# Kernel optimization log

Hardware: AMD Instinct MI355X
Metric: run time of the kernel (lower is better)

The kernel has to match this reference:

```python
import jax, jax.numpy as jnp
import numpy as np
from jax import lax

H = 160; W = 160
D_MODEL = 128; D_INNER = 512; D_STATE = 256; NHEADS = 16; HEADDIM = 32
D_CONV = 4; CHUNK = 64
CONV_DIM = D_INNER + 2 * D_STATE            # 1024
D_IN_PROJ = 2 * D_INNER + 2 * D_STATE + NHEADS  # 1552
EPS = 1e-5


def setup_inputs() -> dict:
    key = jax.random.key(0)
    ks = jax.random.split(key, 8)
    nrm = lambda k, s, sc: jax.random.normal(k, s, jnp.float32) * sc
    return {
        "x": jax.random.normal(ks[0], (1, 3, H, W), jnp.float32),
        "fc0_w": nrm(ks[1], (D_MODEL, 3), 0.3),
        "fc0_b": jnp.zeros((D_MODEL,), jnp.float32),
        "in_proj_w": nrm(ks[2], (D_IN_PROJ, D_MODEL), D_MODEL ** -0.5),
        "conv_w": nrm(ks[3], (CONV_DIM, D_CONV), 0.3),
        "conv_b": jnp.zeros((CONV_DIM,), jnp.float32),
        "dt_bias": jnp.log(jnp.expm1(jax.random.uniform(ks[4], (NHEADS,), minval=0.001, maxval=0.1))),
        "A_log": jnp.log(jax.random.uniform(ks[5], (NHEADS,), minval=1.0, maxval=16.0)),
        "D": jnp.ones((NHEADS,), jnp.float32),
        "norm_w": jnp.ones((D_INNER,), jnp.float32),
        "out_proj_w": nrm(ks[6], (D_MODEL, D_INNER), D_INNER ** -0.5),
        "fc1_w": nrm(ks[7], (D_MODEL, H * W), (H * W) ** -0.5),
        "fc1_b": jnp.zeros((D_MODEL,), jnp.float32),
    }


def segsum(x):
    # x: (..., T) -> (..., T, T) with out[i,j] = sum_{j < d <= i} x[d], -inf above diag
    T = x.shape[-1]
    strict = jnp.tril(jnp.ones((T, T), dtype=bool), -1)
    xx = jnp.where(strict, x[..., :, None], 0.0)
    cs = jnp.cumsum(xx, axis=-2)
    keep = jnp.tril(jnp.ones((T, T), dtype=bool))
    return jnp.where(keep, cs, -jnp.inf)


def ssd(xh, A, Bm, Cm):
    # xh: (b,l,h,p) already multiplied by dt; A: (b,l,h) = dt*A_head; Bm,Cm: (b,l,n) (ngroups=1)
    b, l, h, p = xh.shape
    n = Bm.shape[-1]
    c, q = l // CHUNK, CHUNK
    xh = xh.reshape(b, c, q, h, p)
    A = A.reshape(b, c, q, h).transpose(0, 3, 1, 2)          # (b,h,c,q)
    Bm = Bm.reshape(b, c, q, n)
    Cm = Cm.reshape(b, c, q, n)
    A_cs = jnp.cumsum(A, axis=-1)                            # (b,h,c,q)
    Lmat = jnp.exp(segsum(A))                                # (b,h,c,q,q)
    # intra-chunk (quadratic attention-like) term
    Y_diag = jnp.einsum('bcln,bcsn,bhcls,bcshp->bclhp', Cm, Bm, Lmat, xh)
    # per-chunk final states
    decay = jnp.exp(A_cs[..., -1:] - A_cs)                   # (b,h,c,q)
    states = jnp.einsum('bcln,bhcl,bclhp->bchpn', Bm, decay, xh)
    # inter-chunk recurrence: state entering each chunk
    a_tot = jnp.exp(A_cs[..., -1])                           # (b,h,c)
    def step(carry, inp):
        a_c, s_c = inp                                       # (b,h), (b,h,p,n)
        return a_c[..., None, None] * carry + s_c, carry
    _, states_in = lax.scan(step, jnp.zeros((b, h, p, n), xh.dtype),
                            (jnp.moveaxis(a_tot, 2, 0), jnp.moveaxis(states, 1, 0)))
    states_in = jnp.moveaxis(states_in, 0, 1)                # (b,c,h,p,n)
    Y_off = jnp.einsum('bcln,bchpn,bhcl->bclhp', Cm, states_in, jnp.exp(A_cs))
    return (Y_diag + Y_off).reshape(b, l, h, p)


def _forward(x, fc0_w, fc0_b, in_proj_w, conv_w, conv_b, dt_bias, A_log, D,
             norm_w, out_proj_w, fc1_w, fc1_b):
    b = x.shape[0]
    hw = H * W
    # bidirectional pixel flattening
    x1 = x.transpose(0, 2, 3, 1).reshape(b, hw, 3)
    x2 = x[:, :, ::-1, ::-1].transpose(0, 2, 3, 1).reshape(b, hw, 3)
    xc = jnp.concatenate([x1, x2], axis=1)                   # (b, 2*hw, 3)
    u = xc @ fc0_w.T + fc0_b                                 # (b, L, 128)
    L = u.shape[1]
    # Mamba2 in_proj
    zxbcdt = u @ in_proj_w.T                                 # (b, L, 1552)
    z = zxbcdt[..., :D_INNER]
    xBC = zxbcdt[..., D_INNER:D_INNER + CONV_DIM]
    dt = jax.nn.softplus(zxbcdt[..., D_INNER + CONV_DIM:] + dt_bias)  # (b, L, 16)
    # causal depthwise conv1d + silu
    conv = lax.conv_general_dilated(xBC.transpose(0, 2, 1), conv_w[:, None, :],
                                    (1,), [(D_CONV - 1, 0)],
                                    feature_group_count=CONV_DIM,
                                    dimension_numbers=('NCH', 'OIH', 'NCH'))
    xBC = jax.nn.silu(conv + conv_b[None, :, None]).transpose(0, 2, 1)
    xh = xBC[..., :D_INNER].reshape(b, L, NHEADS, HEADDIM)
    Bm = xBC[..., D_INNER:D_INNER + D_STATE]
    Cm = xBC[..., D_INNER + D_STATE:]
    A = -jnp.exp(A_log)                                      # (16,)
    Y = ssd(xh * dt[..., None], dt * A, Bm, Cm)
    Y = Y + D[None, None, :, None] * xh                      # skip connection
    y = Y.reshape(b, L, D_INNER)
    # gated RMSNorm (norm_before_gate=False)
    y = y * jax.nn.silu(z)
    y = y * lax.rsqrt(jnp.mean(y * y, axis=-1, keepdims=True) + EPS) * norm_w
    out = y @ out_proj_w.T                                   # (b, L, 128)
    # second half of sequence, mean over feature dim (AdaptiveAvgPool1d(1))
    half = out[:, hw:, :].mean(axis=-1)                      # (b, hw)
    return half @ fc1_w.T + fc1_b                            # (b, 128)


def reference(x, fc0_w, fc0_b, in_proj_w, conv_w, conv_b, dt_bias, A_log, D,
              norm_w, out_proj_w, fc1_w, fc1_b):
    return _forward(x, fc0_w, fc0_b, in_proj_w, conv_w, conv_b, dt_bias, A_log,
                    D, norm_w, out_proj_w, fc1_w, fc1_b)
```

## Files before the change

### kernel.cpp

```cpp
#include <hip/hip_runtime.h>

#define H_ 160
#define W_ 160
#define HW 25600
#define L_ 51200
#define DM 128
#define DI 512
#define DS 256
#define NH 16
#define HD 32
#define CONVD 1024
#define DIP 1552
#define NCH 800
#define NCH2 400
#define HPB 8
#define KSL 32
#define CPS 13
#define EPSV 1e-5f

typedef __attribute__((ext_vector_type(8))) short bf16x8;
typedef __attribute__((ext_vector_type(8))) unsigned short us8;
typedef __attribute__((ext_vector_type(4))) unsigned short us4;
typedef __attribute__((ext_vector_type(4))) float f32x4;
#define MFMA16(a,b,c) __builtin_amdgcn_mfma_f32_16x16x32_bf16(a,b,c,0,0,0)

__device__ __forceinline__ float b2f(unsigned short u){
  union{unsigned int i; float f;} v; v.i = ((unsigned int)u) << 16; return v.f;
}
__device__ __forceinline__ unsigned short f2b(float f){
  union{unsigned int i; float f;} v; v.f = f;
  unsigned int r = v.i + 0x7fffu + ((v.i >> 16) & 1u);
  return (unsigned short)(r >> 16);
}

__global__ void k_coef(const float* __restrict__ opw, const float* __restrict__ nw,
                       float* __restrict__ coef){
  int i = blockIdx.x * blockDim.x + threadIdx.x;
  if (i >= DI) return;
  float s = 0.f;
  for (int j = 0; j < DM; ++j) s += opw[j * DI + i];
  coef[i] = (s / (float)DM) * nw[i];
}

__global__ __launch_bounds__(256) void k_qtab(const float* __restrict__ ipw,
    const float* __restrict__ fw, const float* __restrict__ fb, float* __restrict__ q){
  int j = blockIdx.x * 256 + threadIdx.x;
  if (j >= DIP) return;
  const float* wr = ipw + (size_t)j * DM;
  float s0 = 0.f, s1 = 0.f, s2 = 0.f, sb = 0.f;
  for (int k = 0; k < DM; ++k){
    float w = wr[k];
    s0 += w * fw[k*3+0]; s1 += w * fw[k*3+1]; s2 += w * fw[k*3+2]; sb += w * fb[k];
  }
  reinterpret_cast<float4*>(q)[j] = make_float4(s0, s1, s2, sb);
}

__device__ __forceinline__ void xrow(const float* __restrict__ x, int l, float* o){
  int i, j;
  if (l < HW){ i = l / W_; j = l % W_; }
  else { int l2 = l - HW; i = (H_ - 1) - l2 / W_; j = (W_ - 1) - l2 % W_; }
  int p = i * W_ + j;
  o[0] = x[p]; o[1] = x[HW + p]; o[2] = x[2*HW + p];
}

__global__ __launch_bounds__(256) void k_fused(const float* __restrict__ x,
    const float* __restrict__ q, const float* __restrict__ cw, const float* __restrict__ cb,
    const float* __restrict__ dt_bias,
    unsigned short* __restrict__ g, unsigned short* __restrict__ xbc, float* __restrict__ dtb){
  int r0 = blockIdx.x * 32;
  int tid = threadIdx.x;
  {
    int c8 = tid & 127, lg = tid >> 7;
    const float4* qv8 = reinterpret_cast<const float4*>(q) + DI + c8 * 8;
    const float4* wv8 = reinterpret_cast<const float4*>(cw) + c8 * 8;
    const float4* cb2 = reinterpret_cast<const float4*>(cb) + c8 * 2;
    float4 bias0 = cb2[0], bias1 = cb2[1];
    float biasv[8] = {bias0.x,bias0.y,bias0.z,bias0.w,bias1.x,bias1.y,bias1.z,bias1.w};
    for (int it = 0; it < 4; ++it){
      int lbase = r0 + (it * 2 + lg) * 4;
      float xv[7][3], vf[7];
      #pragma unroll
      for (int k = 0; k < 7; ++k){
        int l = lbase - 3 + k;
        if (l >= 0){ xrow(x, l, xv[k]); vf[k] = 1.f; }
        else { xv[k][0] = xv[k][1] = xv[k][2] = 0.f; vf[k] = 0.f; }
      }
      unsigned int ow[4][4];
      #pragma unroll
      for (int e = 0; e < 8; ++e){
        float4 qv = qv8[e];
        float raw[7];
        #pragma unroll
        for (int k = 0; k < 7; ++k)
          raw[k] = vf[k]*qv.w + xv[k][0]*qv.x + xv[k][1]*qv.y + xv[k][2]*qv.z;
        float4 wv = wv8[e];
        float bias = biasv[e];
        #pragma unroll
        for (int rr = 0; rr < 4; ++rr){
          float acc = bias + raw[rr]*wv.x + raw[rr+1]*wv.y + raw[rr+2]*wv.z + raw[rr+3]*wv.w;
          float s = acc / (1.f + __expf(-acc));
          unsigned int b = f2b(s);
          if (e & 1) ow[rr][e >> 1] |= b << 16;
          else       ow[rr][e >> 1] = b;
        }
      }
      #pragma unroll
      for (int rr = 0; rr < 4; ++rr){
        uint4 o; o.x = ow[rr][0]; o.y = ow[rr][1]; o.z = ow[rr][2]; o.w = ow[rr][3];
        *reinterpret_cast<uint4*>(xbc + (size_t)(lbase + rr) * CONVD + c8 * 8) = o;
      }
    }
  }
  if (r0 >= HW){
    int c8g = tid & 63;
    const float4* qv8 = reinterpret_cast<const float4*>(q) + c8g * 8;
    for (int it = 0; it < 8; ++it){
      int row = it * 4 + (tid >> 6);
      int l = r0 + row;
      float xv[3]; xrow(x, l, xv);
      unsigned int ow[4];
      #pragma unroll
      for (int e = 0; e < 8; ++e){
        float4 qv = qv8[e];
        float raw = qv.w + xv[0]*qv.x + xv[1]*qv.y + xv[2]*qv.z;
        float s = raw / (1.f + __expf(-raw));
        unsigned int b = f2b(s);
        if (e & 1) ow[e >> 1] |= b << 16;
        else       ow[e >> 1] = b;
      }
      uint4 o; o.x = ow[0]; o.y = ow[1]; o.z = ow[2]; o.w = ow[3];
      *reinterpret_cast<uint4*>(g + (size_t)(l - HW) * DI + c8g * 8) = o;
    }
  }
  {
    int row = tid >> 3, h2 = (tid & 7) * 2;
    int l = r0 + row;
    float xv[3]; xrow(x, l, xv);
    #pragma unroll
    for (int e = 0; e < 2; ++e){
      int h = h2 + e;
      float4 qv = reinterpret_cast<const float4*>(q)[DI + CONVD + h];
      float raw = qv.w + xv[0]*qv.x + xv[1]*qv.y + xv[2]*qv.z + dt_bias[h];
      float sp = (raw > 20.f) ? raw : log1pf(__expf(raw));
      dtb[(size_t)l * NH + h] = sp;
    }
  }
}

__global__ void k_csum(const float* __restrict__ dtb, const float* __restrict__ A_log,
                       float* __restrict__ Scs){
  int idx = blockIdx.x * 256 + threadIdx.x;
  if (idx >= NCH2 * NH) return;
  int c = idx >> 4, h = idx & 15;
  float Ah = -__expf(A_log[h]);
  float s = 0.f;
  const float* p = dtb + (size_t)c * 64 * NH + h;
  for (int t = 0; t < 64; ++t) s += p[t * NH];
  Scs[idx] = s * Ah;
}

__global__ __launch_bounds__(256) void k_cpre(const float* __restrict__ Scs,
    float* __restrict__ chunkpre, float* __restrict__ Ttot){
  __shared__ float segs[256];
  int tid = threadIdx.x;
  int h = tid & 15, seg = tid >> 4;
  int c0 = seg * 25;
  float v[25];
  float s = 0.f;
  #pragma unroll
  for (int j = 0; j < 25; ++j){ v[j] = Scs[(c0 + j) * NH + h]; s += v[j]; }
  segs[seg * 16 + h] = s;
  __syncthreads();
  float excl = 0.f;
  for (int s2 = 0; s2 < seg; ++s2) excl += segs[s2 * 16 + h];
  float run = excl;
  #pragma unroll
  for (int j = 0; j < 25; ++j){ chunkpre[(c0 + j) * NH + h] = run; run += v[j]; }
  if (seg == 15) Ttot[h] = run;
}

__global__ __launch_bounds__(256) void k_carry(const unsigned short* __restrict__ xbc,
    const float* __restrict__ dtb, const float* __restrict__ A_log,
    const float* __restrict__ chunkpre, const float* __restrict__ Ttot,
    float* __restrict__ part){
  __shared__ char U[37120];
  unsigned short* Bs = (unsigned short*)U;
  char* xwT = U + 32768;
  float* wcs = (float*)(U + 36864);
  int h = blockIdx.x & 15, ks = blockIdx.x >> 4;
  int tid = threadIdx.x, lane = tid & 63, wv = tid >> 6;
  int kg = lane >> 4, l15 = lane & 15;
  int c0 = ks * CPS, cend = min(c0 + CPS, NCH2);
  float Ah = -__expf(A_log[h]);
  float Tt = Ttot[h];
  f32x4 sacc[2][4];
  #pragma unroll
  for (int mt = 0; mt < 2; ++mt)
    #pragma unroll
    for (int nt = 0; nt < 4; ++nt) sacc[mt][nt] = (f32x4){0.f,0.f,0.f,0.f};
  for (int c = c0; c < cend; ++c){
    int l0 = c * 64;
    __syncthreads();
    #pragma unroll
    for (int it = 0; it < 8; ++it){
      int r = (tid >> 5) + 8 * it, c8 = tid & 31;
      uint4 v = *reinterpret_cast<const uint4*>(xbc + (size_t)(l0 + r) * CONVD + DI + c8 * 8);
      *reinterpret_cast<uint4*>((char*)Bs + ((r * 512 + c8 * 16) ^ ((r & 7) << 4))) = v;
    }
    if (wv == 0){
      float d = dtb[(size_t)(l0 + lane) * NH + h] * Ah;
      #pragma unroll
      for (int off = 1; off < 64; off <<= 1){
        float o = __shfl_up(d, off, 64);
        if (lane >= off) d += o;
      }
      wcs[lane] = __expf(Tt - chunkpre[c * NH + h] - d);
    }
    __syncthreads();
    {
      int t = lane, pb = wv;
      float w = wcs[t] * dtb[(size_t)(l0 + t) * NH + h];
      us8 x8 = *reinterpret_cast<const us8*>(xbc + (size_t)(l0 + t) * CONVD + h * HD + pb * 8);
      #pragma unroll
      for (int e = 0; e < 8; ++e){
        int pp = pb * 8 + e;
        *reinterpret_cast<unsigned short*>(xwT + ((pp * 128 + t * 2) ^ ((pp & 7) << 4))) = f2b(b2f(x8[e]) * w);
      }
    }
    __syncthreads();
    #pragma unroll
    for (int s = 0; s < 2; ++s){
      bf16x8 bfr[4];
      #pragma unroll
      for (int nt = 0; nt < 4; ++nt){
        int n = wv * 64 + nt * 16 + l15;
        bf16x8 f;
        #pragma unroll
        for (int e = 0; e < 8; ++e){
          int t = s * 32 + kg * 8 + e;
          f[e] = *reinterpret_cast<const short*>((char*)Bs + ((t * 512 + n * 2) ^ ((t & 7) << 4)));
        }
        bfr[nt] = f;
      }
      #pragma unroll
      for (int mt = 0; mt < 2; ++mt){
        int pr = mt * 16 + l15;
        bf16x8 a = *reinterpret_cast<const bf16x8*>(xwT + ((pr * 128 + (s*32 + kg*8) * 2) ^ ((pr & 7) << 4)));
        #pragma unroll
        for (int nt = 0; nt < 4; ++nt) sacc[mt][nt] = MFMA16(a, bfr[nt], sacc[mt][nt]);
      }
    }
  }
  float* pb2 = part + ((size_t)(ks * NH + h)) * HD * DS;
  #pragma unroll
  for (int mt = 0; mt < 2; ++mt)
    #pragma unroll
    for (int nt = 0; nt < 4; ++nt)
      #pragma unroll
      for (int r = 0; r < 4; ++r)
        pb2[(mt * 16 + kg * 4 + r) * DS + wv * 64 + nt * 16 + l15] = sacc[mt][nt][r];
}

__global__ __launch_bounds__(256) void k_carryred(const float* __restrict__ part,
                                                  float* __restrict__ carry){
  int idx = blockIdx.x * 256 + threadIdx.x;
  float s = 0.f;
  #pragma unroll 8
  for (int ks = 0; ks < KSL; ++ks) s += part[(size_t)ks * 131072 + idx];
  carry[idx] = s;
}

__global__ __launch_bounds__(256) void k_chunk(const unsigned short* __restrict__ xbc,
    const float* __restrict__ dtb, const float* __restrict__ A_log,
    unsigned short* __restrict__ states, float* __restrict__ atot,
    float* __restrict__ ecs, unsigned short* __restrict__ ydiag){
  __shared__ char U[65536];
  __shared__ float dts[64 * HPB];
  __shared__ float Acs[HPB * 64];
  unsigned short* Bs = (unsigned short*)U;
  unsigned short* Cs = (unsigned short*)(U + 32768);
  char* Mb  = U;
  char* xdT = U + 8192;
  char* xwT = U + 12288;
  unsigned short* stageS = (unsigned short*)(U + 16384);
  unsigned short* stageY = (unsigned short*)(U + 33280);
  int cl = blockIdx.x >> 1, hg = blockIdx.x & 1;
  int hbase = hg * HPB;
  int c = NCH2 + cl, l0 = c * 64;
  int tid = threadIdx.x, lane = tid & 63, wv = tid >> 6;
  int kg = lane >> 4, l15 = lane & 15;

  for (int i = tid; i < 64 * HPB; i += 256){
    int t = i >> 3, hh = i & 7;
    dts[i] = dtb[(size_t)(l0 + t) * NH + hbase + hh];
  }
  #pragma unroll
  for (int it = 0; it < 8; ++it){
    int r = (tid >> 5) + 8 * it, c8 = tid & 31;
    uint4 v = *reinterpret_cast<const uint4*>(xbc + (size_t)(l0 + r) * CONVD + DI + c8 * 8);
    *reinterpret_cast<uint4*>((char*)Bs + ((r * 512 + c8 * 16) ^ ((r & 7) << 4))) = v;
    uint4 v2 = *reinterpret_cast<const uint4*>(xbc + (size_t)(l0 + r) * CONVD + DI + DS + c8 * 8);
    *reinterpret_cast<uint4*>((char*)Cs + ((r * 512 + c8 * 16) ^ ((r & 7) << 4))) = v2;
  }
  __syncthreads();
  if (tid < HPB){
    int hh = tid; float Ah = -__expf(A_log[hbase + hh]); float s = 0.f;
    for (int t = 0; t < 64; ++t){ s += dts[t*HPB + hh] * Ah; Acs[hh*64 + t] = s; }
    atot[c * NH + hbase + hh] = __expf(s);
  }
  bf16x8 bst[8];
  #pragma unroll
  for (int nt = 0; nt < 4; ++nt)
    #pragma unroll
    for (int s = 0; s < 2; ++s){
      int n = wv * 64 + nt * 16 + l15;
      int tb = s * 32 + kg * 8;
      bf16x8 f;
      #pragma unroll
      for (int e = 0; e < 8; ++e){
        int t = tb + e;
        f[e] = *reinterpret_cast<const short*>((char*)Bs + ((t * 512 + n * 2) ^ ((t & 7) << 4)));
      }
      bst[nt * 2 + s] = f;
    }
  f32x4 Gacc[4];
  {
    #pragma unroll
    for (int st = 0; st < 4; ++st) Gacc[st] = (f32x4){0.f,0.f,0.f,0.f};
    int trow = wv * 16 + l15;
    for (int ks = 0; ks < 8; ++ks){
      bf16x8 a = *reinterpret_cast<const bf16x8*>((char*)Cs + ((trow * 512 + (ks*32 + kg*8) * 2) ^ ((trow & 7) << 4)));
      #pragma unroll
      for (int st = 0; st < 4; ++st){
        int srow = st * 16 + l15;
        bf16x8 b = *reinterpret_cast<const bf16x8*>((char*)Bs + ((srow * 512 + (ks*32 + kg*8) * 2) ^ ((srow & 7) << 4)));
        Gacc[st] = MFMA16(a, b, Gacc[st]);
      }
    }
  }
  __syncthreads();
  for (int hh = 0; hh < HPB; ++hh){
    int h = hbase + hh;
    float alast = Acs[hh*64 + 63];
    {
      int t = tid & 63, pb = tid >> 6;
      float dtv = dts[t*HPB + hh];
      float dec = __expf(alast - Acs[hh*64 + t]);
      us8 x8 = *reinterpret_cast<const us8*>(xbc + (size_t)(l0 + t) * CONVD + h * HD + pb * 8);
      #pragma unroll
      for (int e = 0; e < 8; ++e){
        int pp = pb * 8 + e;
        float v = b2f(x8[e]) * dtv;
        *reinterpret_cast<unsigned short*>(xdT + ((pp * 128 + t * 2) ^ ((pp & 7) << 4))) = f2b(v);
        *reinterpret_cast<unsigned short*>(xwT + ((pp * 128 + t * 2) ^ ((pp & 7) << 4))) = f2b(v * dec);
      }
    }
    {
      #pragma unroll
      for (int st = 0; st < 4; ++st)
        #pragma unroll
        for (int r = 0; r < 4; ++r){
          int t = wv * 16 + kg * 4 + r, s2 = st * 16 + l15;
          float m = (s2 <= t) ? Gacc[st][r] * __expf(Acs[hh*64 + t] - Acs[hh*64 + s2]) : 0.f;
          *reinterpret_cast<unsigned short*>(Mb + ((t * 128 + s2 * 2) ^ ((t & 7) << 4))) = f2b(m);
        }
      if (tid < 64) ecs[((size_t)cl * NH + h) * 64 + tid] = __expf(Acs[hh*64 + tid]);
    }
    __syncthreads();
    {
      f32x4 sacc[2][4];
      #pragma unroll
      for (int mt = 0; mt < 2; ++mt)
        #pragma unroll
        for (int nt = 0; nt < 4; ++nt) sacc[mt][nt] = (f32x4){0.f,0.f,0.f,0.f};
      #pragma unroll
      for (int s = 0; s < 2; ++s)
        #pragma unroll
        for (int mt = 0; mt < 2; ++mt){
          int pr = mt * 16 + l15;
          bf16x8 a = *reinterpret_cast<const bf16x8*>(xwT + ((pr * 128 + (s*32 + kg*8) * 2) ^ ((pr & 7) << 4)));
          #pragma unroll
          for (int nt = 0; nt < 4; ++nt) sacc[mt][nt] = MFMA16(a, bst[nt*2 + s], sacc[mt][nt]);
        }
      #pragma unroll
      for (int mt = 0; mt < 2; ++mt)
        #pragma unroll
        for (int nt = 0; nt < 4; ++nt)
          #pragma unroll
          for (int r = 0; r < 4; ++r){
            int pp = mt * 16 + kg * 4 + r, n = wv * 64 + nt * 16 + l15;
            stageS[pp * 264 + n] = f2b(sacc[mt][nt][r]);
          }
    }
    {
      f32x4 yacc[2];
      yacc[0] = (f32x4){0.f,0.f,0.f,0.f}; yacc[1] = (f32x4){0.f,0.f,0.f,0.f};
      int trow = wv * 16 + l15;
      #pragma unroll
      for (int s = 0; s < 2; ++s){
        bf16x8 a = *reinterpret_cast<const bf16x8*>(Mb + ((trow * 128 + (s*32 + kg*8) * 2) ^ ((trow & 7) << 4)));
        #pragma unroll
        for (int pt = 0; pt < 2; ++pt){
          int pr = pt * 16 + l15;
          bf16x8 b = *reinterpret_cast<const bf16x8*>(xdT + ((pr * 128 + (s*32 + kg*8) * 2) ^ ((pr & 7) << 4)));
          yacc[pt] = MFMA16(a, b, yacc[pt]);
        }
      }
      #pragma unroll
      for (int pt = 0; pt < 2; ++pt)
        #pragma unroll
        for (int r = 0; r < 4; ++r){
          int t = wv * 16 + kg * 4 + r, pp = pt * 16 + l15;
          stageY[t * 40 + pp] = f2b(yacc[pt][r]);
        }
    }
    __syncthreads();
    {
      int row = tid >> 3, seg = tid & 7;
      const unsigned short* sp = stageS + row * 264 + seg * 32;
      unsigned short* gp = states + (((size_t)cl * NH + h) * HD + row) * DS + seg * 32;
      #pragma unroll
      for (int k = 0; k < 4; ++k)
        *reinterpret_cast<uint4*>(gp + k * 8) = *reinterpret_cast<const uint4*>(sp + k * 8);
      {
        int rw = tid >> 2, quad = tid & 3;
        *reinterpret_cast<uint4*>(ydiag + (size_t)(l0 - HW + rw) * DI + h * HD + quad * 8)
          = *reinterpret_cast<const uint4*>(stageY + rw * 40 + quad * 8);
      }
    }
    __syncthreads();
  }
}

__global__ __launch_bounds__(256) void k_scan2(unsigned short* __restrict__ states,
    const float* __restrict__ atot, const float* __restrict__ carry){
  __shared__ float sat[NCH2];
  int idx = blockIdx.x * 256 + threadIdx.x;
  int h = idx >> 13;
  for (int c = threadIdx.x; c < NCH2; c += 256) sat[c] = atot[(NCH2 + c) * NH + h];
  __syncthreads();
  float cr = carry[idx];
  unsigned short* p = states + idx;
  for (int c = 0; c < NCH2; ++c){
    float s = b2f(*p);
    *p = f2b(cr);
    cr = sat[c] * cr + s;
    p += 131072;
  }
}

__global__ __launch_bounds__(256) void k_yoff(const unsigned short* __restrict__ xbc,
    const unsigned short* __restrict__ states, const float* __restrict__ ecs,
    const float* __restrict__ Dv, unsigned short* __restrict__ y,
    const unsigned short* __restrict__ g, float* __restrict__ rms){
  __shared__ unsigned short stage[64 * 520];
  __shared__ float ecs_s[1024];
  int c2 = blockIdx.x;
  int c = c2 + NCH2, l0 = c * 64;
  int tid = threadIdx.x, lane = tid & 63, wv = tid >> 6;
  int kg = lane >> 4, l15 = lane & 15;
  for (int i = tid; i < 1024; i += 256) ecs_s[i] = ecs[(size_t)c2 * 1024 + i];
  bf16x8 aC[8];
  int trow = wv * 16 + l15;
  #pragma unroll
  for (int ks = 0; ks < 8; ++ks)
    aC[ks] = *reinterpret_cast<const bf16x8*>(xbc + (size_t)(l0 + trow) * CONVD + DI + DS + ks * 32 + kg * 8);
  __syncthreads();
  for (int h = 0; h < NH; ++h){
    f32x4 acc[2];
    acc[0] = (f32x4){0.f,0.f,0.f,0.f}; acc[1] = (f32x4){0.f,0.f,0.f,0.f};
    const unsigned short* sb = states + ((size_t)c2 * NH + h) * HD * DS;
    #pragma unroll
    for (int ks = 0; ks < 8; ++ks)
      #pragma unroll
      for (int pt = 0; pt < 2; ++pt){
        bf16x8 b = *reinterpret_cast<const bf16x8*>(sb + (pt * 16 + l15) * DS + ks * 32 + kg * 8);
        acc[pt] = MFMA16(aC[ks], b, acc[pt]);
      }
    float Dh = Dv[h];
    #pragma unroll
    for (int pt = 0; pt < 2; ++pt)
      #pragma unroll
      for (int r = 0; r < 4; ++r){
        int t = wv * 16 + kg * 4 + r, pp = pt * 16 + l15;
        float xh = b2f(xbc[(size_t)(l0 + t) * CONVD + h * HD + pp]);
        stage[t * 520 + h * HD + pp] = f2b(ecs_s[h*64 + t] * acc[pt][r] + Dh * xh);
      }
  }
  __syncthreads();
  int row = tid >> 2, quad = tid & 3;
  const unsigned short* sr = stage + row * 520 + quad * 128;
  size_t obase = (size_t)(c2 * 64 + row) * DI + quad * 128;
  float ss = 0.f;
  #pragma unroll
  for (int k = 0; k < 16; ++k){
    uint4 sv = *reinterpret_cast<const uint4*>(sr + k * 8);
    uint4 yv = *reinterpret_cast<const uint4*>(y + obase + k * 8);
    uint4 gv = *reinterpret_cast<const uint4*>(g + obase + k * 8);
    unsigned int ow[4];
    const unsigned int* svp = (const unsigned int*)&sv;
    const unsigned int* yvp = (const unsigned int*)&yv;
    const unsigned int* gvp = (const unsigned int*)&gv;
    #pragma unroll
    for (int e = 0; e < 4; ++e){
      float v0 = b2f((unsigned short)(svp[e] & 0xffff)) + b2f((unsigned short)(yvp[e] & 0xffff));
      float v1 = b2f((unsigned short)(svp[e] >> 16)) + b2f((unsigned short)(yvp[e] >> 16));
      float y0 = v0 * b2f((unsigned short)(gvp[e] & 0xffff));
      float y1 = v1 * b2f((unsigned short)(gvp[e] >> 16));
      ss += y0 * y0 + y1 * y1;
      ow[e] = (unsigned int)f2b(y0) | ((unsigned int)f2b(y1) << 16);
    }
    uint4 o; o.x = ow[0]; o.y = ow[1]; o.z = ow[2]; o.w = ow[3];
    *reinterpret_cast<uint4*>(y + obase + k * 8) = o;
  }
  ss += __shfl_xor(ss, 1, 64);
  ss += __shfl_xor(ss, 2, 64);
  if (quad == 0) rms[c2 * 64 + row] = rsqrtf(ss / (float)DI + EPSV);
}

__global__ __launch_bounds__(256) void k_half(const unsigned short* __restrict__ yg,
    const float* __restrict__ rms, const float* __restrict__ coef,
    float* __restrict__ half_out){
  int wave = threadIdx.x >> 6, lane = threadIdx.x & 63;
  int row = blockIdx.x * 4 + wave;
  if (row >= HW) return;
  const unsigned short* yr = yg + (size_t)row * DI;
  float acc = 0.f;
  for (int i = lane; i < DI; i += 64) acc += b2f(yr[i]) * coef[i];
  #pragma unroll
  for (int off = 32; off; off >>= 1) acc += __shfl_down(acc, off, 64);
  if (lane == 0) half_out[row] = acc * rms[row];
}

__global__ __launch_bounds__(256) void k_fc1(const float* __restrict__ half_in,
    const float* __restrict__ w, const float* __restrict__ b, float* __restrict__ out){
  int k = blockIdx.x;
  const float* wr = w + (size_t)k * HW;
  float acc = 0.f;
  for (int i = threadIdx.x; i < HW; i += 256) acc += half_in[i] * wr[i];
  __shared__ float red[256];
  red[threadIdx.x] = acc;
  __syncthreads();
  for (int s = 128; s; s >>= 1){
    if (threadIdx.x < s) red[threadIdx.x] += red[threadIdx.x + s];
    __syncthreads();
  }
  if (threadIdx.x == 0) out[k] = red[0] + b[k];
}

extern "C" void kernel_launch(void* const* d_in, const int* in_sizes, int n_in,
                              void* d_out, int out_size, void* d_ws, size_t ws_size,
                              hipStream_t stream){
  const float* x      = (const float*)d_in[0];
  const float* fc0_w  = (const float*)d_in[1];
  const float* fc0_b  = (const float*)d_in[2];
  const float* ipw    = (const float*)d_in[3];
  const float* conv_w = (const float*)d_in[4];
  const float* conv_b = (const float*)d_in[5];
  const float* dt_bias= (const float*)d_in[6];
  const float* A_log  = (const float*)d_in[7];
  const float* Dv     = (const float*)d_in[8];
  const float* norm_w = (const float*)d_in[9];
  const float* opw    = (const float*)d_in[10];
  const float* fc1_w  = (const float*)d_in[11];
  const float* fc1_b  = (const float*)d_in[12];
  float* out = (float*)d_out;

  char* ws = (char*)d_ws;
  size_t off = 0;
  float* dtb          = (float*)(ws + off);           off += (size_t)L_ * NH * 4;
  unsigned short* stx = (unsigned short*)(ws + off);  off += (size_t)L_ * CONVD * 2;
  unsigned short* xbc = (unsigned short*)(ws + off);  off += (size_t)L_ * CONVD * 2;
  unsigned short* g   = (unsigned short*)(ws + off);  off += (size_t)HW * DI * 2;
  unsigned short* yd  = (unsigned short*)(ws + off);  off += (size_t)HW * DI * 2;
  float* atot         = (float*)(ws + off);           off += (size_t)NCH * NH * 4;
  float* ecs          = (float*)(ws + off);           off += (size_t)NCH2 * NH * 64 * 4;
  float* rms          = (float*)(ws + off);           off += (size_t)HW * 4;
  float* half_buf     = (float*)(ws + off);           off += (size_t)HW * 4;
  float* coef         = (float*)(ws + off);           off += (size_t)DI * 4;
  float* carry        = (float*)(ws + off);           off += (size_t)131072 * 4;
  float* qtab         = (float*)(ws + off);           off += (size_t)DIP * 4 * 4;
  float* Scs          = (float*)(ws + off);           off += (size_t)NCH2 * NH * 4;
  float* chunkpre     = (float*)(ws + off);           off += (size_t)NCH2 * NH * 4;
  float* Ttot         = (float*)(ws + off);           off += (size_t)NH * 4;
  float* part         = (float*)stx;

  if (ws_size < off) return;

  k_coef    <<<2, 256, 0, stream>>>(opw, norm_w, coef);
  k_qtab    <<<(DIP + 255) / 256, 256, 0, stream>>>(ipw, fc0_w, fc0_b, qtab);
  k_fused   <<<L_ / 32, 256, 0, stream>>>(x, qtab, conv_w, conv_b, dt_bias, g, xbc, dtb);
  k_csum    <<<25, 256, 0, stream>>>(dtb, A_log, Scs);
  k_cpre    <<<1, 256, 0, stream>>>(Scs, chunkpre, Ttot);
  k_carry   <<<KSL * NH, 256, 0, stream>>>(xbc, dtb, A_log, chunkpre, Ttot, part);
  k_carryred<<<512, 256, 0, stream>>>(part, carry);
  k_chunk   <<<NCH2 * 2, 256, 0, stream>>>(xbc, dtb, A_log, stx, atot, ecs, yd);
  k_scan2   <<<512, 256, 0, stream>>>(stx, atot, carry);
  k_yoff    <<<NCH2, 256, 0, stream>>>(xbc, stx, ecs, Dv, yd, g, rms);
  k_half    <<<HW / 4, 256, 0, stream>>>(yd, rms, coef, half_buf);
  k_fc1     <<<DM, 256, 0, stream>>>(half_buf, fc1_w, fc1_b, out);
}
```

Baseline: 501.3 us.

## Rebalance fused, carry and chunk kernels for head-grouped operand reuse

k_carry now processes four heads per block, loading B fragments once and reusing them across heads, and doubles the number of K-slices. k_chunk handles all 16 heads in one block, so the per-chunk B/C staging and Gram computation are shared rather than duplicated across two head groups. k_fused splits channels across two blocks and spreads the gate rows over all blocks to balance work. The gains come from fewer redundant loads and better balance, at the cost of larger accumulator register footprint and half as many k_chunk blocks.

```diff
diff --git a/kernel.cpp b/kernel.cpp
--- a/kernel.cpp
+++ b/kernel.cpp
@@ -13,9 +13,8 @@
 #define DIP 1552
 #define NCH 800
 #define NCH2 400
-#define HPB 8
-#define KSL 32
-#define CPS 13
+#define KSL 64
+#define CPS 7
 #define EPSV 1e-5f
 
 typedef __attribute__((ext_vector_type(8))) short bf16x8;
@@ -67,17 +66,20 @@
     const float* __restrict__ q, const float* __restrict__ cw, const float* __restrict__ cb,
     const float* __restrict__ dt_bias,
     unsigned short* __restrict__ g, unsigned short* __restrict__ xbc, float* __restrict__ dtb){
-  int r0 = blockIdx.x * 32;
+  int bid = blockIdx.x;
+  int r0 = (bid >> 1) * 32;
+  int chalf = bid & 1;
   int tid = threadIdx.x;
   {
-    int c8 = tid & 127, lg = tid >> 7;
+    int c8 = (tid & 63) | (chalf << 6);
+    int lg = tid >> 6;
     const float4* qv8 = reinterpret_cast<const float4*>(q) + DI + c8 * 8;
     const float4* wv8 = reinterpret_cast<const float4*>(cw) + c8 * 8;
     const float4* cb2 = reinterpret_cast<const float4*>(cb) + c8 * 2;
     float4 bias0 = cb2[0], bias1 = cb2[1];
     float biasv[8] = {bias0.x,bias0.y,bias0.z,bias0.w,bias1.x,bias1.y,bias1.z,bias1.w};
-    for (int it = 0; it < 4; ++it){
-      int lbase = r0 + (it * 2 + lg) * 4;
+    for (int it = 0; it < 2; ++it){
+      int lbase = r0 + (it * 4 + lg) * 4;
       float xv[7][3], vf[7];
       #pragma unroll
       for (int k = 0; k < 7; ++k){
@@ -111,12 +113,12 @@
       }
     }
   }
-  if (r0 >= HW){
+  {
     int c8g = tid & 63;
     const float4* qv8 = reinterpret_cast<const float4*>(q) + c8g * 8;
-    for (int it = 0; it < 8; ++it){
+    for (int it = 0; it < 2; ++it){
       int row = it * 4 + (tid >> 6);
-      int l = r0 + row;
+      int l = HW + bid * 8 + row;
       float xv[3]; xrow(x, l, xv);
       unsigned int ow[4];
       #pragma unroll
@@ -129,21 +131,17 @@
         else       ow[e >> 1] = b;
       }
       uint4 o; o.x = ow[0]; o.y = ow[1]; o.z = ow[2]; o.w = ow[3];
-      *reinterpret_cast<uint4*>(g + (size_t)(l - HW) * DI + c8g * 8) = o;
+      *reinterpret_cast<uint4*>(g + (size_t)(bid * 8 + row) * DI + c8g * 8) = o;
     }
   }
   {
-    int row = tid >> 3, h2 = (tid & 7) * 2;
-    int l = r0 + row;
+    int row = tid >> 4, h = tid & 15;
+    int l = r0 + chalf * 16 + row;
     float xv[3]; xrow(x, l, xv);
-    #pragma unroll
-    for (int e = 0; e < 2; ++e){
-      int h = h2 + e;
-      float4 qv = reinterpret_cast<const float4*>(q)[DI + CONVD + h];
-      float raw = qv.w + xv[0]*qv.x + xv[1]*qv.y + xv[2]*qv.z + dt_bias[h];
-      float sp = (raw > 20.f) ? raw : log1pf(__expf(raw));
-      dtb[(size_t)l * NH + h] = sp;
-    }
+    float4 qv = reinterpret_cast<const float4*>(q)[DI + CONVD + h];
+    float raw = qv.w + xv[0]*qv.x + xv[1]*qv.y + xv[2]*qv.z + dt_bias[h];
+    float sp = (raw > 20.f) ? raw : log1pf(__expf(raw));
+    dtb[(size_t)l * NH + h] = sp;
   }
 }
 
@@ -183,21 +181,24 @@
     const float* __restrict__ dtb, const float* __restrict__ A_log,
     const float* __restrict__ chunkpre, const float* __restrict__ Ttot,
     float* __restrict__ part){
-  __shared__ char U[37120];
+  __shared__ char U[50176];
   unsigned short* Bs = (unsigned short*)U;
-  char* xwT = U + 32768;
-  float* wcs = (float*)(U + 36864);
-  int h = blockIdx.x & 15, ks = blockIdx.x >> 4;
+  char* xwT4 = U + 32768;
+  float* wcs = (float*)(U + 49152);
+  int ks = blockIdx.x >> 2, hg = blockIdx.x & 3;
+  int hbase = hg * 4;
   int tid = threadIdx.x, lane = tid & 63, wv = tid >> 6;
   int kg = lane >> 4, l15 = lane & 15;
   int c0 = ks * CPS, cend = min(c0 + CPS, NCH2);
-  float Ah = -__expf(A_log[h]);
-  float Tt = Ttot[h];
-  f32x4 sacc[2][4];
-  #pragma unroll
-  for (int mt = 0; mt < 2; ++mt)
-    #pragma unroll
-    for (int nt = 0; nt < 4; ++nt) sacc[mt][nt] = (f32x4){0.f,0.f,0.f,0.f};
+  float Ahw = -__expf(A_log[hbase + wv]);
+  float Ttw = Ttot[hbase + wv];
+  f32x4 sacc[4][2][4];
+  #pragma unroll
+  for (int hh = 0; hh < 4; ++hh)
+    #pragma unroll
+    for (int mt = 0; mt < 2; ++mt)
+      #pragma unroll
+      for (int nt = 0; nt < 4; ++nt) sacc[hh][mt][nt] = (f32x4){0.f,0.f,0.f,0.f};
   for (int c = c0; c < cend; ++c){
     int l0 = c * 64;
     __syncthreads();
@@ -207,58 +208,66 @@
       uint4 v = *reinterpret_cast<const uint4*>(xbc + (size_t)(l0 + r) * CONVD + DI + c8 * 8);
       *reinterpret_cast<uint4*>((char*)Bs + ((r * 512 + c8 * 16) ^ ((r & 7) << 4))) = v;
     }
-    if (wv == 0){
-      float d = dtb[(size_t)(l0 + lane) * NH + h] * Ah;
+    {
+      float d = dtb[(size_t)(l0 + lane) * NH + hbase + wv] * Ahw;
       #pragma unroll
       for (int off = 1; off < 64; off <<= 1){
         float o = __shfl_up(d, off, 64);
         if (lane >= off) d += o;
       }
-      wcs[lane] = __expf(Tt - chunkpre[c * NH + h] - d);
+      wcs[wv * 64 + lane] = __expf(Ttw - chunkpre[c * NH + hbase + wv] - d);
     }
     __syncthreads();
-    {
+    bf16x8 bst[8];
+    #pragma unroll
+    for (int nt = 0; nt < 4; ++nt)
+      #pragma unroll
+      for (int s = 0; s < 2; ++s){
+        int n = wv * 64 + nt * 16 + l15;
+        int tb = s * 32 + kg * 8;
+        bf16x8 f;
+        #pragma unroll
+        for (int e = 0; e < 8; ++e){
+          int t = tb + e;
+          f[e] = *reinterpret_cast<const short*>((char*)Bs + ((t * 512 + n * 2) ^ ((t & 7) << 4)));
+        }
+        bst[nt * 2 + s] = f;
+      }
+    #pragma unroll
+    for (int hh = 0; hh < 4; ++hh){
       int t = lane, pb = wv;
-      float w = wcs[t] * dtb[(size_t)(l0 + t) * NH + h];
-      us8 x8 = *reinterpret_cast<const us8*>(xbc + (size_t)(l0 + t) * CONVD + h * HD + pb * 8);
+      float w = wcs[hh * 64 + t] * dtb[(size_t)(l0 + t) * NH + hbase + hh];
+      us8 x8 = *reinterpret_cast<const us8*>(xbc + (size_t)(l0 + t) * CONVD + (hbase + hh) * HD + pb * 8);
       #pragma unroll
       for (int e = 0; e < 8; ++e){
         int pp = pb * 8 + e;
-        *reinterpret_cast<unsigned short*>(xwT + ((pp * 128 + t * 2) ^ ((pp & 7) << 4))) = f2b(b2f(x8[e]) * w);
+        *reinterpret_cast<unsigned short*>(xwT4 + hh * 4096 + ((pp * 128 + t * 2) ^ ((pp & 7) << 4))) = f2b(b2f(x8[e]) * w);
       }
     }
     __syncthreads();
     #pragma unroll
-    for (int s = 0; s < 2; ++s){
-      bf16x8 bfr[4];
-      #pragma unroll
-      for (int nt = 0; nt < 4; ++nt){
-        int n = wv * 64 + nt * 16 + l15;
-        bf16x8 f;
-        #pragma unroll
-        for (int e = 0; e < 8; ++e){
-          int t = s * 32 + kg * 8 + e;
-          f[e] = *reinterpret_cast<const short*>((char*)Bs + ((t * 512 + n * 2) ^ ((t & 7) << 4)));
+    for (int s = 0; s < 2; ++s)
+      #pragma unroll
+      for (int hh = 0; hh < 4; ++hh)
+        #pragma unroll
+        for (int mt = 0; mt < 2; ++mt){
+          int pr = mt * 16 + l15;
+          bf16x8 a = *reinterpret_cast<const bf16x8*>(xwT4 + hh * 4096 + ((pr * 128 + (s*32 + kg*8) * 2) ^ ((pr & 7) << 4)));
+          #pragma unroll
+          for (int nt = 0; nt < 4; ++nt) sacc[hh][mt][nt] = MFMA16(a, bst[nt*2 + s], sacc[hh][mt][nt]);
         }
-        bfr[nt] = f;
-      }
-      #pragma unroll
-      for (int mt = 0; mt < 2; ++mt){
-        int pr = mt * 16 + l15;
-        bf16x8 a = *reinterpret_cast<const bf16x8*>(xwT + ((pr * 128 + (s*32 + kg*8) * 2) ^ ((pr & 7) << 4)));
-        #pragma unroll
-        for (int nt = 0; nt < 4; ++nt) sacc[mt][nt] = MFMA16(a, bfr[nt], sacc[mt][nt]);
-      }
-    }
-  }
-  float* pb2 = part + ((size_t)(ks * NH + h)) * HD * DS;
-  #pragma unroll
-  for (int mt = 0; mt < 2; ++mt)
-    #pragma unroll
-    for (int nt = 0; nt < 4; ++nt)
-      #pragma unroll
-      for (int r = 0; r < 4; ++r)
-        pb2[(mt * 16 + kg * 4 + r) * DS + wv * 64 + nt * 16 + l15] = sacc[mt][nt][r];
+  }
+  #pragma unroll
+  for (int hh = 0; hh < 4; ++hh){
+    float* pb2 = part + ((size_t)(ks * NH + hbase + hh)) * HD * DS;
+    #pragma unroll
+    for (int mt = 0; mt < 2; ++mt)
+      #pragma unroll
+      for (int nt = 0; nt < 4; ++nt)
+        #pragma unroll
+        for (int r = 0; r < 4; ++r)
+          pb2[(mt * 16 + kg * 4 + r) * DS + wv * 64 + nt * 16 + l15] = sacc[hh][mt][nt][r];
+  }
 }
 
 __global__ __launch_bounds__(256) void k_carryred(const float* __restrict__ part,
@@ -275,8 +284,8 @@
     unsigned short* __restrict__ states, float* __restrict__ atot,
     float* __restrict__ ecs, unsigned short* __restrict__ ydiag){
   __shared__ char U[65536];
-  __shared__ float dts[64 * HPB];
-  __shared__ float Acs[HPB * 64];
+  __shared__ float dts[1024];
+  __shared__ float Acs[1024];
   unsigned short* Bs = (unsigned short*)U;
   unsigned short* Cs = (unsigned short*)(U + 32768);
   char* Mb  = U;
@@ -284,16 +293,12 @@
   char* xwT = U + 12288;
   unsigned short* stageS = (unsigned short*)(U + 16384);
   unsigned short* stageY = (unsigned short*)(U + 33280);
-  int cl = blockIdx.x >> 1, hg = blockIdx.x & 1;
-  int hbase = hg * HPB;
+  int cl = blockIdx.x;
   int c = NCH2 + cl, l0 = c * 64;
   int tid = threadIdx.x, lane = tid & 63, wv = tid >> 6;
   int kg = lane >> 4, l15 = lane & 15;
 
-  for (int i = tid; i < 64 * HPB; i += 256){
-    int t = i >> 3, hh = i & 7;
-    dts[i] = dtb[(size_t)(l0 + t) * NH + hbase + hh];
-  }
+  for (int i = tid; i < 1024; i += 256) dts[i] = dtb[(size_t)l0 * NH + i];
   #pragma unroll
   for (int it = 0; it < 8; ++it){
     int r = (tid >> 5) + 8 * it, c8 = tid & 31;
@@ -303,10 +308,10 @@
     *reinterpret_cast<uint4*>((char*)Cs + ((r * 512 + c8 * 16) ^ ((r & 7) << 4))) = v2;
   }
   __syncthreads();
-  if (tid < HPB){
-    int hh = tid; float Ah = -__expf(A_log[hbase + hh]); float s = 0.f;
-    for (int t = 0; t < 64; ++t){ s += dts[t*HPB + hh] * Ah; Acs[hh*64 + t] = s; }
-    atot[c * NH + hbase + hh] = __expf(s);
+  if (tid < 16){
+    int h = tid; float Ah = -__expf(A_log[h]); float s = 0.f;
+    for (int t = 0; t < 64; ++t){ s += dts[t*16 + h] * Ah; Acs[h*64 + t] = s; }
+    atot[c * NH + h] = __expf(s);
   }
   bf16x8 bst[8];
   #pragma unroll
@@ -339,13 +344,12 @@
     }
   }
   __syncthreads();
-  for (int hh = 0; hh < HPB; ++hh){
-    int h = hbase + hh;
-    float alast = Acs[hh*64 + 63];
+  for (int h = 0; h < NH; ++h){
+    float alast = Acs[h*64 + 63];
     {
       int t = tid & 63, pb = tid >> 6;
-      float dtv = dts[t*HPB + hh];
-      float dec = __expf(alast - Acs[hh*64 + t]);
+      float dtv = dts[t*16 + h];
+      float dec = __expf(alast - Acs[h*64 + t]);
       us8 x8 = *reinterpret_cast<const us8*>(xbc + (size_t)(l0 + t) * CONVD + h * HD + pb * 8);
       #pragma unroll
       for (int e = 0; e < 8; ++e){
@@ -361,10 +365,10 @@
         #pragma unroll
         for (int r = 0; r < 4; ++r){
           int t = wv * 16 + kg * 4 + r, s2 = st * 16 + l15;
-          float m = (s2 <= t) ? Gacc[st][r] * __expf(Acs[hh*64 + t] - Acs[hh*64 + s2]) : 0.f;
+          float m = (s2 <= t) ? Gacc[st][r] * __expf(Acs[h*64 + t] - Acs[h*64 + s2]) : 0.f;
           *reinterpret_cast<unsigned short*>(Mb + ((t * 128 + s2 * 2) ^ ((t & 7) << 4))) = f2b(m);
         }
-      if (tid < 64) ecs[((size_t)cl * NH + h) * 64 + tid] = __expf(Acs[hh*64 + tid]);
+      if (tid < 64) ecs[((size_t)cl * NH + h) * 64 + tid] = __expf(Acs[h*64 + tid]);
     }
     __syncthreads();
     {
@@ -589,12 +593,12 @@
 
   k_coef    <<<2, 256, 0, stream>>>(opw, norm_w, coef);
   k_qtab    <<<(DIP + 255) / 256, 256, 0, stream>>>(ipw, fc0_w, fc0_b, qtab);
-  k_fused   <<<L_ / 32, 256, 0, stream>>>(x, qtab, conv_w, conv_b, dt_bias, g, xbc, dtb);
+  k_fused   <<<L_ / 16, 256, 0, stream>>>(x, qtab, conv_w, conv_b, dt_bias, g, xbc, dtb);
   k_csum    <<<25, 256, 0, stream>>>(dtb, A_log, Scs);
   k_cpre    <<<1, 256, 0, stream>>>(Scs, chunkpre, Ttot);
-  k_carry   <<<KSL * NH, 256, 0, stream>>>(xbc, dtb, A_log, chunkpre, Ttot, part);
+  k_carry   <<<KSL * 4, 256, 0, stream>>>(xbc, dtb, A_log, chunkpre, Ttot, part);
   k_carryred<<<512, 256, 0, stream>>>(part, carry);
-  k_chunk   <<<NCH2 * 2, 256, 0, stream>>>(xbc, dtb, A_log, stx, atot, ecs, yd);
+  k_chunk   <<<NCH2, 256, 0, stream>>>(xbc, dtb, A_log, stx, atot, ecs, yd);
   k_scan2   <<<512, 256, 0, stream>>>(stx, atot, carry);
   k_yoff    <<<NCH2, 256, 0, stream>>>(xbc, stx, ecs, Dv, yd, g, rms);
   k_half    <<<HW / 4, 256, 0, stream>>>(yd, rms, coef, half_buf);
```

Result: slower. 534.3 us (+6.6%).
